# Kernel tuning notes

Hardware: AMD Instinct MI355X
Metric: run time of the kernel (lower is better)

Reference implementation:

```python
import jax, jax.numpy as jnp
import numpy as np

NUM_HEADS = 16
THETA = 10000.0


def _rope(x):
    # x: [b, h, s, d_k], interleaved-pair RoPE
    s, d = x.shape[-2], x.shape[-1]
    inv_freq = 1.0 / (THETA ** (jnp.arange(0, d, 2, dtype=jnp.float32) / d))  # [d/2]
    ang = jnp.arange(s, dtype=jnp.float32)[:, None] * inv_freq[None, :]       # [s, d/2]
    cos = jnp.repeat(jnp.cos(ang), 2, axis=-1)[None, None]                    # [1,1,s,d]
    sin = jnp.repeat(jnp.sin(ang), 2, axis=-1)[None, None]
    x_even = x[..., 0::2]
    x_odd = x[..., 1::2]
    rot = jnp.stack((-x_odd, x_even), axis=-1).reshape(x.shape)
    return x * cos.astype(x.dtype) + rot * sin.astype(x.dtype)


def setup_inputs() -> dict:
    key = jax.random.key(0)
    ks = jax.random.split(key, 5)
    b, s, d = 4, 2048, 1024
    std = (2.0 / (d + d)) ** 0.5
    return {
        "x": jax.random.normal(ks[0], (b, s, d), dtype=jnp.float32),
        "wq": jax.random.normal(ks[1], (d, d), dtype=jnp.float32) * std,
        "wk": jax.random.normal(ks[2], (d, d), dtype=jnp.float32) * std,
        "wv": jax.random.normal(ks[3], (d, d), dtype=jnp.float32) * std,
        "wo": jax.random.normal(ks[4], (d, d), dtype=jnp.float32) * std,
    }


def reference(x, wq, wk, wv, wo):
    b, s, d_model = x.shape
    h = NUM_HEADS
    d_k = d_model // h

    def proj(w):
        y = jnp.einsum('bsd,od->bso', x, w)
        return y.reshape(b, s, h, d_k).transpose(0, 2, 1, 3)  # [b,h,s,d_k]

    q = _rope(proj(wq))
    k = _rope(proj(wk))
    v = proj(wv)

    scores = jnp.einsum('bhqd,bhkd->bhqk', q, k) / (d_k ** 0.5)
    causal = jnp.tril(jnp.ones((s, s), dtype=bool))[None, None]
    scores = jnp.where(causal, scores, -jnp.inf)
    attn = jax.nn.softmax(scores, axis=-1)
    out = jnp.einsum('bhqk,bhkd->bhqd', attn, v)
    out = out.transpose(0, 2, 1, 3).reshape(b, s, d_model)
    return jnp.einsum('bsd,od->bso', out, wo)
```

## Files before the change

### kernel.cpp

```cpp
#include <hip/hip_runtime.h>
#include <stdint.h>

#define NHEAD  16
#define SEQ    2048
#define DMODEL 1024
#define BATCH  4

typedef __attribute__((ext_vector_type(4))) float f32x4;
typedef __attribute__((ext_vector_type(8))) __bf16 bf16x8;
typedef __attribute__((ext_vector_type(8))) unsigned short u16x8;

__device__ __forceinline__ unsigned short f2bf(float f) {
    unsigned int u = __builtin_bit_cast(unsigned int, f);
    u += 0x7FFFu + ((u >> 16) & 1u);
    return (unsigned short)(u >> 16);
}

__device__ __forceinline__ unsigned int cvt_pk_bf16(float lo, float hi) {
    unsigned int r;
    asm("v_cvt_pk_bf16_f32 %0, %1, %2" : "=v"(r) : "v"(lo), "v"(hi));
    return r;
}

__device__ __forceinline__ void gload_lds16(const void* g, void* l) {
    __builtin_amdgcn_global_load_lds(
        (const __attribute__((address_space(1))) unsigned int*)(uintptr_t)g,
        (__attribute__((address_space(3))) unsigned int*)(uintptr_t)l,
        16, 0, 0);
}

__device__ __forceinline__ bf16x8 lds_frag(const unsigned short* p) {
    return __builtin_bit_cast(bf16x8, *(const u16x8*)p);
}

__device__ __forceinline__ bf16x8 gfrag(const unsigned short* p) {
    return __builtin_bit_cast(bf16x8, *(const u16x8*)p);
}

__global__ __launch_bounds__(256) void cvt_f32_bf16(const float* __restrict__ src,
                                                    unsigned short* __restrict__ dst, int n4) {
    int i = blockIdx.x * 256 + threadIdx.x;
    if (i < n4) {
        float4 v = ((const float4*)src)[i];
        ushort4 o;
        o.x = f2bf(v.x); o.y = f2bf(v.y); o.z = f2bf(v.z); o.w = f2bf(v.w);
        ((ushort4*)dst)[i] = o;
    }
}

__global__ __launch_bounds__(256) void cvt_weights(const float* __restrict__ w0,
                                                   const float* __restrict__ w1,
                                                   const float* __restrict__ w2,
                                                   const float* __restrict__ w3,
                                                   unsigned short* __restrict__ dst) {
    int which = blockIdx.x >> 10;
    int i = (blockIdx.x & 1023) * 256 + threadIdx.x;
    const float* src = which == 0 ? w0 : which == 1 ? w1 : which == 2 ? w2 : w3;
    unsigned short* d = dst + (size_t)which * 1024 * 1024;
    float4 v = ((const float4*)src)[i];
    ushort4 o;
    o.x = f2bf(v.x); o.y = f2bf(v.y); o.z = f2bf(v.z); o.w = f2bf(v.w);
    ((ushort4*)d)[i] = o;
}

__global__ __launch_bounds__(256) void gemm_qkv(const unsigned short* __restrict__ A,
                                                const unsigned short* __restrict__ Wc,
                                                unsigned short* __restrict__ qw,
                                                unsigned short* __restrict__ kw,
                                                unsigned short* __restrict__ vw) {
    __shared__ __align__(16) unsigned short As[2][128 * 64];
    __shared__ __align__(16) unsigned short Bs[2][128 * 64];

    const int tid  = threadIdx.x;
    const int lane = tid & 63;
    const int wid  = tid >> 6;
    const int wm = wid >> 1, wn = wid & 1;
    const int l15 = lane & 15, lg = lane >> 4;

    const int tn = blockIdx.x;
    const int m0 = blockIdx.y * 128, n0 = tn * 128;

    f32x4 acc[4][4];
#pragma unroll
    for (int i = 0; i < 4; i++)
#pragma unroll
        for (int j = 0; j < 4; j++) acc[i][j] = f32x4{0.f, 0.f, 0.f, 0.f};

    const int e0 = tid * 8;
    auto STAGE = [&](int kk, int bufi) {
#pragma unroll
        for (int is = 0; is < 4; ++is) {
            int e = is * 2048 + e0;
            int row = e >> 6, col = e & 63;
            gload_lds16(A  + (size_t)(m0 + row) * 1024 + kk + col, &As[bufi][e]);
            gload_lds16(Wc + (size_t)(n0 + row) * 1024 + kk + col, &Bs[bufi][e]);
        }
    };

    STAGE(0, 0);
    __syncthreads();

    for (int kk = 0; kk < 1024; kk += 64) {
        const int cur = (kk >> 6) & 1;
        if (kk + 64 < 1024) STAGE(kk + 64, cur ^ 1);
#pragma unroll
        for (int ks = 0; ks < 2; ++ks) {
            bf16x8 a[4], b[4];
#pragma unroll
            for (int f = 0; f < 4; f++) {
                a[f] = lds_frag(&As[cur][(wm * 64 + f * 16 + l15) * 64 + ks * 32 + lg * 8]);
                b[f] = lds_frag(&Bs[cur][(wn * 64 + f * 16 + l15) * 64 + ks * 32 + lg * 8]);
            }
#pragma unroll
            for (int i = 0; i < 4; i++)
#pragma unroll
                for (int j = 0; j < 4; j++)
                    acc[i][j] = __builtin_amdgcn_mfma_f32_16x16x32_bf16(a[i], b[j], acc[i][j], 0, 0, 0);
        }
        __syncthreads();
    }

    if (tn >= 16) {
        unsigned short* out = vw;
#pragma unroll
        for (int i = 0; i < 4; i++)
#pragma unroll
            for (int r = 0; r < 4; r++) {
                int m = m0 + wm * 64 + i * 16 + lg * 4 + r;
                int b = m >> 11, s = m & 2047;
#pragma unroll
                for (int j = 0; j < 4; j++) {
                    int n = n0 + wn * 64 + j * 16 + l15;
                    int h = (n >> 6) & 15, dk = n & 63;
                    out[((size_t)(b * NHEAD + h) * 64 + dk) * SEQ + s] = f2bf(acc[i][j][r]);
                }
            }
    } else {
        unsigned short* out = (tn < 8) ? qw : kw;
        const float qscale = (tn < 8) ? 0.18033688011112042f : 1.0f;
        const float L2T = 13.287712379549449f;
        float invf[4];
#pragma unroll
        for (int j = 0; j < 4; j++) {
            int idx = j * 16 + l15;
            int t = idx >> 1;
            invf[j] = exp2f(-((float)(2 * t) * (1.0f / 64.0f)) * L2T);
        }
        const int par = l15 & 1;
#pragma unroll
        for (int i = 0; i < 4; i++)
#pragma unroll
            for (int r = 0; r < 4; r++) {
                int m = m0 + wm * 64 + i * 16 + lg * 4 + r;
                int b = m >> 11, s = m & 2047;
                float fs = (float)s;
#pragma unroll
                for (int j = 0; j < 4; j++) {
                    float v = acc[i][j][r];
                    float other = __shfl_xor(v, 1);
                    float sn, cs;
                    __sincosf(fs * invf[j], &sn, &cs);
                    float y = par ? fmaf(v, cs, other * sn) : fmaf(v, cs, -other * sn);
                    y *= qscale;
                    int n = n0 + wn * 64 + j * 16 + l15;
                    int h = (n >> 6) & 15, dk = n & 63;
                    out[((size_t)(b * NHEAD + h) * SEQ + s) * 64 + dk] = f2bf(y);
                }
            }
    }
}

__global__ __launch_bounds__(256) void gemm_out(const unsigned short* __restrict__ A,
                                                const unsigned short* __restrict__ W,
                                                float* __restrict__ out) {
    __shared__ __align__(16) unsigned short As[2][128 * 64];
    __shared__ __align__(16) unsigned short Bs[2][128 * 64];

    const int tid  = threadIdx.x;
    const int lane = tid & 63;
    const int wid  = tid >> 6;
    const int wm = wid >> 1, wn = wid & 1;
    const int l15 = lane & 15, lg = lane >> 4;

    const int tn = blockIdx.x & 7;
    const int tm = blockIdx.x >> 3;
    const int m0 = tm * 128, n0 = tn * 128;

    f32x4 acc[4][4];
#pragma unroll
    for (int i = 0; i < 4; i++)
#pragma unroll
        for (int j = 0; j < 4; j++) acc[i][j] = f32x4{0.f, 0.f, 0.f, 0.f};

    const int e0 = tid * 8;
    auto STAGE = [&](int kk, int bufi) {
#pragma unroll
        for (int is = 0; is < 4; ++is) {
            int e = is * 2048 + e0;
            int row = e >> 6, col = e & 63;
            gload_lds16(A + (size_t)(m0 + row) * 1024 + kk + col, &As[bufi][e]);
            gload_lds16(W + (size_t)(n0 + row) * 1024 + kk + col, &Bs[bufi][e]);
        }
    };

    STAGE(0, 0);
    __syncthreads();

    for (int kk = 0; kk < 1024; kk += 64) {
        const int cur = (kk >> 6) & 1;
        if (kk + 64 < 1024) STAGE(kk + 64, cur ^ 1);
#pragma unroll
        for (int ks = 0; ks < 2; ++ks) {
            bf16x8 a[4], b[4];
#pragma unroll
            for (int f = 0; f < 4; f++) {
                a[f] = lds_frag(&As[cur][(wm * 64 + f * 16 + l15) * 64 + ks * 32 + lg * 8]);
                b[f] = lds_frag(&Bs[cur][(wn * 64 + f * 16 + l15) * 64 + ks * 32 + lg * 8]);
            }
#pragma unroll
            for (int i = 0; i < 4; i++)
#pragma unroll
                for (int j = 0; j < 4; j++)
                    acc[i][j] = __builtin_amdgcn_mfma_f32_16x16x32_bf16(a[i], b[j], acc[i][j], 0, 0, 0);
        }
        __syncthreads();
    }

#pragma unroll
    for (int i = 0; i < 4; i++)
#pragma unroll
        for (int r = 0; r < 4; r++) {
            int m = m0 + wm * 64 + i * 16 + lg * 4 + r;
            float* orow = out + (size_t)m * 1024 + n0 + wn * 64 + l15;
#pragma unroll
            for (int j = 0; j < 4; j++) orow[j * 16] = acc[i][j][r];
        }
}

__global__ __launch_bounds__(256, 4) void flash_attn(const unsigned short* __restrict__ Qw,
                                                     const unsigned short* __restrict__ Kw,
                                                     const unsigned short* __restrict__ Vw,
                                                     unsigned short* __restrict__ Ow) {
    __shared__ __align__(16) unsigned short Ks[2][64 * 64];
    __shared__ __align__(16) unsigned short Vs[2][64 * 64];
    __shared__ __align__(16) unsigned short Ps[64 * 64];

    const int tid  = threadIdx.x;
    const int lane = tid & 63;
    const int w    = tid >> 6;
    const int l15 = lane & 15, lg = lane >> 4;
    const int l7 = l15 & 7;

    const int logical = (blockIdx.x & 7) * 128 + (blockIdx.x >> 3);
    const int bh = logical >> 4;
    const int p  = logical & 15;
    const int qbB = 31 - p;
    const int ktmax = qbB;

    const unsigned short* Kbh = Kw + (size_t)bh * (SEQ * 64);
    const unsigned short* Vbh = Vw + (size_t)bh * (64 * SEQ);

    const int qrow0 = w * 16;
    const int prow  = qrow0 + l15;

    const unsigned short* QrowA = Qw + (size_t)bh * (SEQ * 64) + (size_t)(p * 64 + prow) * 64;
    const unsigned short* QrowB = Qw + (size_t)bh * (SEQ * 64) + (size_t)(qbB * 64 + prow) * 64;
    bf16x8 qA0 = gfrag(QrowA + lg * 8), qA1 = gfrag(QrowA + 32 + lg * 8);
    bf16x8 qB0 = gfrag(QrowB + lg * 8), qB1 = gfrag(QrowB + 32 + lg * 8);

    auto STAGE = [&](int kt2, int bufi) {
#pragma unroll
        for (int is = 0; is < 2; ++is) {
            int e = (is * 256 + tid) * 8;
            int row = e >> 6, c = (e >> 3) & 7;
            int sc = (c ^ (row & 7)) << 3;
            gload_lds16(Kbh + (size_t)kt2 * 4096 + row * 64 + sc, &Ks[bufi][e]);
            gload_lds16(Vbh + (size_t)row * SEQ + kt2 * 64 + sc, &Vs[bufi][e]);
        }
    };

    STAGE(0, 0);

    f32x4 oaccA[4], oaccB[4];
#pragma unroll
    for (int f = 0; f < 4; f++) { oaccA[f] = f32x4{0.f, 0.f, 0.f, 0.f}; oaccB[f] = f32x4{0.f, 0.f, 0.f, 0.f}; }
    float mA = -3.0e38f, lA = 0.f, mB = -3.0e38f, lB = 0.f;

    unsigned short* pbase = &Ps[prow * 64];
    const unsigned short* prd = &Ps[prow * 64];

    __syncthreads();

    for (int kt = 0; kt <= ktmax; ++kt) {
        const int cur = kt & 1;
        if (kt < ktmax) STAGE(kt + 1, cur ^ 1);

        auto PROC = [&](bf16x8 q0, bf16x8 q1, f32x4* oacc, float& mrun, float& lrun, bool diag) {
            f32x4 st[4];
#pragma unroll
            for (int f = 0; f < 4; f++) st[f] = f32x4{0.f, 0.f, 0.f, 0.f};
            __builtin_amdgcn_s_setprio(1);
#pragma unroll
            for (int ks = 0; ks < 2; ++ks) {
                bf16x8 qk = (ks == 0) ? q0 : q1;
#pragma unroll
                for (int f = 0; f < 4; f++) {
                    bf16x8 kfrag = lds_frag(&Ks[cur][(f * 16 + l15) * 64 + (((ks * 4 + lg) ^ l7) << 3)]);
                    st[f] = __builtin_amdgcn_mfma_f32_16x16x32_bf16(kfrag, qk, st[f], 0, 0, 0);
                }
            }
            __builtin_amdgcn_s_setprio(0);

            if (diag) {
#pragma unroll
                for (int f = 0; f < 4; f++)
#pragma unroll
                    for (int r = 0; r < 4; r++) {
                        int kv = f * 16 + 4 * lg + r;
                        if (kv > prow) st[f][r] = -3.0e38f;
                    }
            }

            float pm = fmaxf(fmaxf(fmaxf(st[0][0], st[0][1]), fmaxf(st[0][2], st[0][3])),
                             fmaxf(fmaxf(st[1][0], st[1][1]), fmaxf(st[1][2], st[1][3])));
            pm = fmaxf(pm, fmaxf(fmaxf(fmaxf(st[2][0], st[2][1]), fmaxf(st[2][2], st[2][3])),
                                 fmaxf(fmaxf(st[3][0], st[3][1]), fmaxf(st[3][2], st[3][3]))));
            pm = fmaxf(pm, __shfl_xor(pm, 16));
            pm = fmaxf(pm, __shfl_xor(pm, 32));

            if (!__all(pm - mrun <= 8.0f)) {
                float mnew = fmaxf(mrun, pm);
                float sc0 = exp2f(mrun - mnew);
                mrun = mnew;
                lrun *= sc0;
#pragma unroll
                for (int r = 0; r < 4; r++) {
                    float so = __shfl(sc0, lg * 4 + r);
#pragma unroll
                    for (int f = 0; f < 4; f++) oacc[f][r] *= so;
                }
            }

            float lsum = 0.f;
#pragma unroll
            for (int f = 0; f < 4; f++)
#pragma unroll
                for (int r = 0; r < 4; r++) {
                    float e = exp2f(st[f][r] - mrun);
                    st[f][r] = e;
                    lsum += e;
                }
            lsum += __shfl_xor(lsum, 16);
            lsum += __shfl_xor(lsum, 32);
            lrun += lsum;

            {
                const int halfoff = (lg & 1) << 2;
                const int cbase = lg >> 1;
#pragma unroll
                for (int f = 0; f < 4; f++) {
                    uint2 pw;
                    pw.x = cvt_pk_bf16(st[f][0], st[f][1]);
                    pw.y = cvt_pk_bf16(st[f][2], st[f][3]);
                    *(uint2*)(pbase + (((2 * f + cbase) ^ l7) << 3) + halfoff) = pw;
                }
            }

            __builtin_amdgcn_s_setprio(1);
#pragma unroll
            for (int ks = 0; ks < 2; ++ks) {
                bf16x8 pa = lds_frag(prd + (((ks * 4 + lg) ^ l7) << 3));
#pragma unroll
                for (int f = 0; f < 4; f++) {
                    bf16x8 vb = lds_frag(&Vs[cur][(f * 16 + l15) * 64 + (((ks * 4 + lg) ^ l7) << 3)]);
                    oacc[f] = __builtin_amdgcn_mfma_f32_16x16x32_bf16(pa, vb, oacc[f], 0, 0, 0);
                }
            }
            __builtin_amdgcn_s_setprio(0);
        };

        if (kt <= p) PROC(qA0, qA1, oaccA, mA, lA, kt == p);
        PROC(qB0, qB1, oaccB, mB, lB, kt == ktmax);

        __syncthreads();
    }

    const int b = bh >> 4, h = bh & 15;
#pragma unroll
    for (int r = 0; r < 4; r++) {
        float lrA = __shfl(lA, lg * 4 + r);
        float invA = 1.0f / lrA;
        int sgA = p * 64 + qrow0 + lg * 4 + r;
        unsigned short* orowA = Ow + ((size_t)(b * SEQ + sgA) * DMODEL) + h * 64 + l15;
#pragma unroll
        for (int f = 0; f < 4; f++) orowA[f * 16] = f2bf(oaccA[f][r] * invA);

        float lrB = __shfl(lB, lg * 4 + r);
        float invB = 1.0f / lrB;
        int sgB = qbB * 64 + qrow0 + lg * 4 + r;
        unsigned short* orowB = Ow + ((size_t)(b * SEQ + sgB) * DMODEL) + h * 64 + l15;
#pragma unroll
        for (int f = 0; f < 4; f++) orowB[f * 16] = f2bf(oaccB[f][r] * invB);
    }
}

extern "C" void kernel_launch(void* const* d_in, const int* in_sizes, int n_in,
                              void* d_out, int out_size, void* d_ws, size_t ws_size,
                              hipStream_t stream) {
    const float* x  = (const float*)d_in[0];
    const float* wq = (const float*)d_in[1];
    const float* wk = (const float*)d_in[2];
    const float* wv = (const float*)d_in[3];
    const float* wo = (const float*)d_in[4];

    unsigned short* ws = (unsigned short*)d_ws;
    const size_t MEL = (size_t)8192 * 1024;
    const size_t WEL = (size_t)1024 * 1024;
    unsigned short* xb  = ws;
    unsigned short* wqb = xb + MEL;
    unsigned short* wob = wqb + 3 * WEL;
    unsigned short* qw  = wob + WEL;
    unsigned short* kw  = qw + MEL;
    unsigned short* vw  = kw + MEL;
    unsigned short* ow  = vw + MEL;

    cvt_f32_bf16<<<8192, 256, 0, stream>>>(x, xb, (int)(MEL / 4));
    cvt_weights<<<4096, 256, 0, stream>>>(wq, wk, wv, wo, wqb);

    gemm_qkv<<<dim3(24, 64), 256, 0, stream>>>(xb, wqb, qw, kw, vw);

    flash_attn<<<1024, 256, 0, stream>>>(qw, kw, vw, ow);

    gemm_out<<<512, 256, 0, stream>>>(ow, wob, (float*)d_out);
}
```

Before: 190.0 us.

## Single-buffer GEMM LDS, unify GEMM kernels, interleave two QK^T in attention

The QKV and output projections are merged into one templated GEMM whose LDS tiles are single-buffered: each k-step loads, syncs and computes with no prefetch. This halves shared memory so more blocks can be resident, at the cost of losing load/compute overlap. In flash attention, the per-tile processing is split into QK^T, softmax, P-write and PV stages, and both query blocks' QK^T MFMAs are issued back to back before either softmax. This gives more independent MFMA work per step but raises register pressure.

```diff
diff --git a/kernel.cpp b/kernel.cpp
--- a/kernel.cpp
+++ b/kernel.cpp
@@ -63,13 +63,15 @@
     ((ushort4*)d)[i] = o;
 }
 
-__global__ __launch_bounds__(256) void gemm_qkv(const unsigned short* __restrict__ A,
-                                                const unsigned short* __restrict__ Wc,
-                                                unsigned short* __restrict__ qw,
-                                                unsigned short* __restrict__ kw,
-                                                unsigned short* __restrict__ vw) {
-    __shared__ __align__(16) unsigned short As[2][128 * 64];
-    __shared__ __align__(16) unsigned short Bs[2][128 * 64];
+template <int MODE>
+__global__ __launch_bounds__(256) void gemm128(const unsigned short* __restrict__ A,
+                                               const unsigned short* __restrict__ Wc,
+                                               unsigned short* __restrict__ qw,
+                                               unsigned short* __restrict__ kw,
+                                               unsigned short* __restrict__ vw,
+                                               float* __restrict__ fout) {
+    __shared__ __align__(16) unsigned short As[128 * 64];
+    __shared__ __align__(16) unsigned short Bs[128 * 64];
 
     const int tid  = threadIdx.x;
     const int lane = tid & 63;
@@ -87,29 +89,23 @@
         for (int j = 0; j < 4; j++) acc[i][j] = f32x4{0.f, 0.f, 0.f, 0.f};
 
     const int e0 = tid * 8;
-    auto STAGE = [&](int kk, int bufi) {
+
+    for (int kk = 0; kk < 1024; kk += 64) {
 #pragma unroll
         for (int is = 0; is < 4; ++is) {
             int e = is * 2048 + e0;
             int row = e >> 6, col = e & 63;
-            gload_lds16(A  + (size_t)(m0 + row) * 1024 + kk + col, &As[bufi][e]);
-            gload_lds16(Wc + (size_t)(n0 + row) * 1024 + kk + col, &Bs[bufi][e]);
-        }
-    };
-
-    STAGE(0, 0);
-    __syncthreads();
-
-    for (int kk = 0; kk < 1024; kk += 64) {
-        const int cur = (kk >> 6) & 1;
-        if (kk + 64 < 1024) STAGE(kk + 64, cur ^ 1);
+            gload_lds16(A  + (size_t)(m0 + row) * 1024 + kk + col, &As[e]);
+            gload_lds16(Wc + (size_t)(n0 + row) * 1024 + kk + col, &Bs[e]);
+        }
+        __syncthreads();
 #pragma unroll
         for (int ks = 0; ks < 2; ++ks) {
             bf16x8 a[4], b[4];
 #pragma unroll
             for (int f = 0; f < 4; f++) {
-                a[f] = lds_frag(&As[cur][(wm * 64 + f * 16 + l15) * 64 + ks * 32 + lg * 8]);
-                b[f] = lds_frag(&Bs[cur][(wn * 64 + f * 16 + l15) * 64 + ks * 32 + lg * 8]);
+                a[f] = lds_frag(&As[(wm * 64 + f * 16 + l15) * 64 + ks * 32 + lg * 8]);
+                b[f] = lds_frag(&Bs[(wn * 64 + f * 16 + l15) * 64 + ks * 32 + lg * 8]);
             }
 #pragma unroll
             for (int i = 0; i < 4; i++)
@@ -120,7 +116,18 @@
         __syncthreads();
     }
 
-    if (tn >= 16) {
+    if (MODE == 1) {
+        float* out = fout;
+#pragma unroll
+        for (int i = 0; i < 4; i++)
+#pragma unroll
+            for (int r = 0; r < 4; r++) {
+                int m = m0 + wm * 64 + i * 16 + lg * 4 + r;
+                float* orow = out + (size_t)m * 1024 + n0 + wn * 64 + l15;
+#pragma unroll
+                for (int j = 0; j < 4; j++) orow[j * 16] = acc[i][j][r];
+            }
+    } else if (tn >= 16) {
         unsigned short* out = vw;
 #pragma unroll
         for (int i = 0; i < 4; i++)
@@ -170,73 +177,6 @@
     }
 }
 
-__global__ __launch_bounds__(256) void gemm_out(const unsigned short* __restrict__ A,
-                                                const unsigned short* __restrict__ W,
-                                                float* __restrict__ out) {
-    __shared__ __align__(16) unsigned short As[2][128 * 64];
-    __shared__ __align__(16) unsigned short Bs[2][128 * 64];
-
-    const int tid  = threadIdx.x;
-    const int lane = tid & 63;
-    const int wid  = tid >> 6;
-    const int wm = wid >> 1, wn = wid & 1;
-    const int l15 = lane & 15, lg = lane >> 4;
-
-    const int tn = blockIdx.x & 7;
-    const int tm = blockIdx.x >> 3;
-    const int m0 = tm * 128, n0 = tn * 128;
-
-    f32x4 acc[4][4];
-#pragma unroll
-    for (int i = 0; i < 4; i++)
-#pragma unroll
-        for (int j = 0; j < 4; j++) acc[i][j] = f32x4{0.f, 0.f, 0.f, 0.f};
-
-    const int e0 = tid * 8;
-    auto STAGE = [&](int kk, int bufi) {
-#pragma unroll
-        for (int is = 0; is < 4; ++is) {
-            int e = is * 2048 + e0;
-            int row = e >> 6, col = e & 63;
-            gload_lds16(A + (size_t)(m0 + row) * 1024 + kk + col, &As[bufi][e]);
-            gload_lds16(W + (size_t)(n0 + row) * 1024 + kk + col, &Bs[bufi][e]);
-        }
-    };
-
-    STAGE(0, 0);
-    __syncthreads();
-
-    for (int kk = 0; kk < 1024; kk += 64) {
-        const int cur = (kk >> 6) & 1;
-        if (kk + 64 < 1024) STAGE(kk + 64, cur ^ 1);
-#pragma unroll
-        for (int ks = 0; ks < 2; ++ks) {
-            bf16x8 a[4], b[4];
-#pragma unroll
-            for (int f = 0; f < 4; f++) {
-                a[f] = lds_frag(&As[cur][(wm * 64 + f * 16 + l15) * 64 + ks * 32 + lg * 8]);
-                b[f] = lds_frag(&Bs[cur][(wn * 64 + f * 16 + l15) * 64 + ks * 32 + lg * 8]);
-            }
-#pragma unroll
-            for (int i = 0; i < 4; i++)
-#pragma unroll
-                for (int j = 0; j < 4; j++)
-                    acc[i][j] = __builtin_amdgcn_mfma_f32_16x16x32_bf16(a[i], b[j], acc[i][j], 0, 0, 0);
-        }
-        __syncthreads();
-    }
-
-#pragma unroll
-    for (int i = 0; i < 4; i++)
-#pragma unroll
-        for (int r = 0; r < 4; r++) {
-            int m = m0 + wm * 64 + i * 16 + lg * 4 + r;
-            float* orow = out + (size_t)m * 1024 + n0 + wn * 64 + l15;
-#pragma unroll
-            for (int j = 0; j < 4; j++) orow[j * 16] = acc[i][j][r];
-        }
-}
-
 __global__ __launch_bounds__(256, 4) void flash_attn(const unsigned short* __restrict__ Qw,
                                                      const unsigned short* __restrict__ Kw,
                                                      const unsigned short* __restrict__ Vw,
@@ -289,98 +229,115 @@
     unsigned short* pbase = &Ps[prow * 64];
     const unsigned short* prd = &Ps[prow * 64];
 
+    auto QKT = [&](bf16x8 q0, bf16x8 q1, f32x4* st, int cur) {
+#pragma unroll
+        for (int f = 0; f < 4; f++) st[f] = f32x4{0.f, 0.f, 0.f, 0.f};
+        __builtin_amdgcn_s_setprio(1);
+#pragma unroll
+        for (int ks = 0; ks < 2; ++ks) {
+            bf16x8 qk = (ks == 0) ? q0 : q1;
+#pragma unroll
+            for (int f = 0; f < 4; f++) {
+                bf16x8 kfrag = lds_frag(&Ks[cur][(f * 16 + l15) * 64 + (((ks * 4 + lg) ^ l7) << 3)]);
+                st[f] = __builtin_amdgcn_mfma_f32_16x16x32_bf16(kfrag, qk, st[f], 0, 0, 0);
+            }
+        }
+        __builtin_amdgcn_s_setprio(0);
+    };
+
+    auto SMAX = [&](f32x4* st, f32x4* oacc, float& mrun, float& lrun, bool diag) {
+        if (diag) {
+#pragma unroll
+            for (int f = 0; f < 4; f++)
+#pragma unroll
+                for (int r = 0; r < 4; r++) {
+                    int kv = f * 16 + 4 * lg + r;
+                    if (kv > prow) st[f][r] = -3.0e38f;
+                }
+        }
+        float pm = fmaxf(fmaxf(fmaxf(st[0][0], st[0][1]), fmaxf(st[0][2], st[0][3])),
+                         fmaxf(fmaxf(st[1][0], st[1][1]), fmaxf(st[1][2], st[1][3])));
+        pm = fmaxf(pm, fmaxf(fmaxf(fmaxf(st[2][0], st[2][1]), fmaxf(st[2][2], st[2][3])),
+                             fmaxf(fmaxf(st[3][0], st[3][1]), fmaxf(st[3][2], st[3][3]))));
+        pm = fmaxf(pm, __shfl_xor(pm, 16));
+        pm = fmaxf(pm, __shfl_xor(pm, 32));
+
+        if (!__all(pm - mrun <= 8.0f)) {
+            float mnew = fmaxf(mrun, pm);
+            float sc0 = exp2f(mrun - mnew);
+            mrun = mnew;
+            lrun *= sc0;
+#pragma unroll
+            for (int r = 0; r < 4; r++) {
+                float so = __shfl(sc0, lg * 4 + r);
+#pragma unroll
+                for (int f = 0; f < 4; f++) oacc[f][r] *= so;
+            }
+        }
+
+        float lsum = 0.f;
+#pragma unroll
+        for (int f = 0; f < 4; f++)
+#pragma unroll
+            for (int r = 0; r < 4; r++) {
+                float e = exp2f(st[f][r] - mrun);
+                st[f][r] = e;
+                lsum += e;
+            }
+        lsum += __shfl_xor(lsum, 16);
+        lsum += __shfl_xor(lsum, 32);
+        lrun += lsum;
+    };
+
+    auto PWRITE = [&](f32x4* st) {
+        const int halfoff = (lg & 1) << 2;
+        const int cbase = lg >> 1;
+#pragma unroll
+        for (int f = 0; f < 4; f++) {
+            uint2 pw;
+            pw.x = cvt_pk_bf16(st[f][0], st[f][1]);
+            pw.y = cvt_pk_bf16(st[f][2], st[f][3]);
+            *(uint2*)(pbase + (((2 * f + cbase) ^ l7) << 3) + halfoff) = pw;
+        }
+    };
+
+    auto PV = [&](f32x4* oacc, int cur) {
+        __builtin_amdgcn_s_setprio(1);
+#pragma unroll
+        for (int ks = 0; ks < 2; ++ks) {
+            bf16x8 pa = lds_frag(prd + (((ks * 4 + lg) ^ l7) << 3));
+#pragma unroll
+            for (int f = 0; f < 4; f++) {
+                bf16x8 vb = lds_frag(&Vs[cur][(f * 16 + l15) * 64 + (((ks * 4 + lg) ^ l7) << 3)]);
+                oacc[f] = __builtin_amdgcn_mfma_f32_16x16x32_bf16(pa, vb, oacc[f], 0, 0, 0);
+            }
+        }
+        __builtin_amdgcn_s_setprio(0);
+    };
+
     __syncthreads();
 
     for (int kt = 0; kt <= ktmax; ++kt) {
         const int cur = kt & 1;
         if (kt < ktmax) STAGE(kt + 1, cur ^ 1);
 
-        auto PROC = [&](bf16x8 q0, bf16x8 q1, f32x4* oacc, float& mrun, float& lrun, bool diag) {
-            f32x4 st[4];
-#pragma unroll
-            for (int f = 0; f < 4; f++) st[f] = f32x4{0.f, 0.f, 0.f, 0.f};
-            __builtin_amdgcn_s_setprio(1);
-#pragma unroll
-            for (int ks = 0; ks < 2; ++ks) {
-                bf16x8 qk = (ks == 0) ? q0 : q1;
-#pragma unroll
-                for (int f = 0; f < 4; f++) {
-                    bf16x8 kfrag = lds_frag(&Ks[cur][(f * 16 + l15) * 64 + (((ks * 4 + lg) ^ l7) << 3)]);
-                    st[f] = __builtin_amdgcn_mfma_f32_16x16x32_bf16(kfrag, qk, st[f], 0, 0, 0);
-                }
-            }
-            __builtin_amdgcn_s_setprio(0);
-
-            if (diag) {
-#pragma unroll
-                for (int f = 0; f < 4; f++)
-#pragma unroll
-                    for (int r = 0; r < 4; r++) {
-                        int kv = f * 16 + 4 * lg + r;
-                        if (kv > prow) st[f][r] = -3.0e38f;
-                    }
-            }
-
-            float pm = fmaxf(fmaxf(fmaxf(st[0][0], st[0][1]), fmaxf(st[0][2], st[0][3])),
-                             fmaxf(fmaxf(st[1][0], st[1][1]), fmaxf(st[1][2], st[1][3])));
-            pm = fmaxf(pm, fmaxf(fmaxf(fmaxf(st[2][0], st[2][1]), fmaxf(st[2][2], st[2][3])),
-                                 fmaxf(fmaxf(st[3][0], st[3][1]), fmaxf(st[3][2], st[3][3]))));
-            pm = fmaxf(pm, __shfl_xor(pm, 16));
-            pm = fmaxf(pm, __shfl_xor(pm, 32));
-
-            if (!__all(pm - mrun <= 8.0f)) {
-                float mnew = fmaxf(mrun, pm);
-                float sc0 = exp2f(mrun - mnew);
-                mrun = mnew;
-                lrun *= sc0;
-#pragma unroll
-                for (int r = 0; r < 4; r++) {
-                    float so = __shfl(sc0, lg * 4 + r);
-#pragma unroll
-                    for (int f = 0; f < 4; f++) oacc[f][r] *= so;
-                }
-            }
-
-            float lsum = 0.f;
-#pragma unroll
-            for (int f = 0; f < 4; f++)
-#pragma unroll
-                for (int r = 0; r < 4; r++) {
-                    float e = exp2f(st[f][r] - mrun);
-                    st[f][r] = e;
-                    lsum += e;
-                }
-            lsum += __shfl_xor(lsum, 16);
-            lsum += __shfl_xor(lsum, 32);
-            lrun += lsum;
-
-            {
-                const int halfoff = (lg & 1) << 2;
-                const int cbase = lg >> 1;
-#pragma unroll
-                for (int f = 0; f < 4; f++) {
-                    uint2 pw;
-                    pw.x = cvt_pk_bf16(st[f][0], st[f][1]);
-                    pw.y = cvt_pk_bf16(st[f][2], st[f][3]);
-                    *(uint2*)(pbase + (((2 * f + cbase) ^ l7) << 3) + halfoff) = pw;
-                }
-            }
-
-            __builtin_amdgcn_s_setprio(1);
-#pragma unroll
-            for (int ks = 0; ks < 2; ++ks) {
-                bf16x8 pa = lds_frag(prd + (((ks * 4 + lg) ^ l7) << 3));
-#pragma unroll
-                for (int f = 0; f < 4; f++) {
-                    bf16x8 vb = lds_frag(&Vs[cur][(f * 16 + l15) * 64 + (((ks * 4 + lg) ^ l7) << 3)]);
-                    oacc[f] = __builtin_amdgcn_mfma_f32_16x16x32_bf16(pa, vb, oacc[f], 0, 0, 0);
-                }
-            }
-            __builtin_amdgcn_s_setprio(0);
-        };
-
-        if (kt <= p) PROC(qA0, qA1, oaccA, mA, lA, kt == p);
-        PROC(qB0, qB1, oaccB, mB, lB, kt == ktmax);
+        if (kt <= p) {
+            f32x4 stA[4], stB[4];
+            QKT(qA0, qA1, stA, cur);
+            QKT(qB0, qB1, stB, cur);
+            SMAX(stA, oaccA, mA, lA, kt == p);
+            PWRITE(stA);
+            PV(oaccA, cur);
+            SMAX(stB, oaccB, mB, lB, false);
+            PWRITE(stB);
+            PV(oaccB, cur);
+        } else {
+            f32x4 stB[4];
+            QKT(qB0, qB1, stB, cur);
+            SMAX(stB, oaccB, mB, lB, kt == ktmax);
+            PWRITE(stB);
+            PV(oaccB, cur);
+        }
 
         __syncthreads();
     }
@@ -427,9 +384,9 @@
     cvt_f32_bf16<<<8192, 256, 0, stream>>>(x, xb, (int)(MEL / 4));
     cvt_weights<<<4096, 256, 0, stream>>>(wq, wk, wv, wo, wqb);
 
-    gemm_qkv<<<dim3(24, 64), 256, 0, stream>>>(xb, wqb, qw, kw, vw);
+    gemm128<0><<<dim3(24, 64), 256, 0, stream>>>(xb, wqb, qw, kw, vw, nullptr);
 
     flash_attn<<<1024, 256, 0, stream>>>(qw, kw, vw, ow);
 
-    gemm_out<<<512, 256, 0, stream>>>(ow, wob, (float*)d_out);
-}
+    gemm128<1><<<dim3(8, 64), 256, 0, stream>>>(ow, wob, nullptr, nullptr, nullptr, (float*)d_out);
+}
```

After: 293.5 us. 1.54x slower.
